# Performance work log

Measured on AMD Instinct MI355X. Metric: run time of the kernel, lower is better.

The kernel has to match this reference:

```python
import jax, jax.numpy as jnp
import numpy as np

PATCH = 7
STRIDE = 1


def extract_patches(im, p=PATCH, stride=STRIDE):
    # im: [b, c, h, w] -> patches [b, N, c*p*p] (torch.nn.Unfold-style layout)
    pt = jax.lax.conv_general_dilated_patches(
        im, filter_shape=(p, p), window_strides=(stride, stride), padding='VALID')
    # pt: [b, c*p*p, h', w']
    b, d = pt.shape[0], pt.shape[1]
    return pt.reshape(b, d, -1).transpose(0, 2, 1)  # [b, N, d]


def coherence_swd(xp, yp, rand):
    # xp, yp: [N, d]; rand: [d, P]
    r = rand / jnp.std(rand, axis=0, keepdims=True, ddof=1)  # torch.std is unbiased
    px = xp @ r  # [N, P]
    py = yp @ r  # [N, P]
    ix = jnp.argsort(px, axis=0).T  # [P, N]
    iy = jnp.argsort(py, axis=0).T  # [P, N]
    # Gather full patch vectors by per-projection sorted order, L1 distance.
    # xp[ix]: [P, N, d] -- the big irregular-gather intermediate.
    diff = jnp.abs(xp[ix] - yp[iy])  # [P, N, d]
    # loss = (1/P) * sum_p mean(|...|_p); each term has identical size -> plain mean
    return diff.mean()


def setup_inputs() -> dict:
    key = jax.random.key(0)
    k1, k2, k3 = jax.random.split(key, 3)
    b, c, h, w = 1, 3, 96, 96
    d = c * PATCH * PATCH  # 147
    num_proj = 256
    x = jax.random.normal(k1, (b, c, h, w), dtype=jnp.float32)
    y = jax.random.normal(k2, (b, c, h, w), dtype=jnp.float32)
    rand = jax.random.normal(k3, (d, num_proj), dtype=jnp.float32)
    return {"x": x, "y": y, "rand": rand}


def reference(x, y, rand):
    x_patches = extract_patches(x)  # [b, N, d]
    y_patches = extract_patches(y)
    losses = jax.vmap(coherence_swd, in_axes=(0, 0, None))(x_patches, y_patches, rand)  # [b]
    return losses.mean()  # batch_reduction='mean'
```

## Files before the change

### kernel.cpp

```cpp
#include <hip/hip_runtime.h>

#define HH 96
#define WW 96
#define OH 90
#define OW 90
#define NPATCH 8100
#define DD 147
#define NPROJ 256
#define TN 64
#define KPAD 160
#define NKS 5
#define SORT_T 512
#define NBUCK 4096
#define KPT 16
#define PGRP 16
#define NCH 64
#define KPB2 128

typedef float vf2 __attribute__((ext_vector_type(2)));
typedef short bf16x8 __attribute__((ext_vector_type(8)));
typedef float f32x4 __attribute__((ext_vector_type(4)));

__device__ __forceinline__ unsigned short bf16_rne(float f) {
    unsigned u = __builtin_bit_cast(unsigned, f);
    u += 0x7FFFu + ((u >> 16) & 1u);
    return (unsigned short)(u >> 16);
}
__device__ __forceinline__ float bf16_f(unsigned short h) {
    return __builtin_bit_cast(float, (unsigned)h << 16);
}

__global__ __launch_bounds__(1024)
void prep_rnd_kernel(const float* __restrict__ rnd,
                     unsigned short* __restrict__ rth,
                     unsigned short* __restrict__ rtl)
{
    const int idx = blockIdx.x * 1024 + threadIdx.x;
    const int k = idx >> 8;
    const int p = idx & 255;
    const float v = (k < DD) ? rnd[k * NPROJ + p] : 0.f;
    const unsigned short hi = bf16_rne(v);
    const unsigned short lo = bf16_rne(v - bf16_f(hi));
    rth[p * KPAD + k] = hi;
    rtl[p * KPAD + k] = lo;
}

__global__ __launch_bounds__(512, 4)
void patch_proj_kernel(const float* __restrict__ x, const float* __restrict__ y,
                       const unsigned short* __restrict__ rth,
                       const unsigned short* __restrict__ rtl,
                       int* __restrict__ xm8, int* __restrict__ ym8,
                       int* __restrict__ xt8, int* __restrict__ yt8,
                       float* __restrict__ pxT, float* __restrict__ pyT,
                       float* __restrict__ out)
{
    __shared__ unsigned short sh[2][TN * KPAD];
    const int tid = threadIdx.x;
    const int n0 = blockIdx.x * TN;
    const int img = blockIdx.y;
    const float* __restrict__ src = img ? y : x;
    int* __restrict__ m8 = img ? ym8 : xm8;
    int* __restrict__ t8 = img ? yt8 : xt8;
    float* __restrict__ pT = img ? pyT : pxT;
    if (blockIdx.x == 0 && img == 0 && tid == 0) out[0] = 0.0f;

    for (int idx = tid; idx < TN * KPAD; idx += 512) {
        const int t = idx / KPAD;
        const int d = idx - t * KPAD;
        const int n = n0 + t;
        float v = 0.f;
        if (n < NPATCH && d < DD) {
            const int oy = n / OW, ox = n - oy * OW;
            const int c  = d / 49, r  = d - c * 49;
            const int di = r / 7,  dj = r - di * 7;
            v = src[c * (HH * WW) + (oy + di) * WW + (ox + dj)];
        }
        const unsigned short hi = bf16_rne(v);
        const unsigned short lo = bf16_rne(v - bf16_f(hi));
        const int mt = t >> 4, r16 = t & 15;
        const int ks = d >> 5, q = (d & 31) >> 3, j = d & 7;
        const int fidx = (((mt * NKS + ks) * 4 + q) * 16 + r16) * 8 + j;
        sh[0][fidx] = hi;
        sh[1][fidx] = lo;
    }
    __syncthreads();

    for (int idx = tid; idx < TN * 40; idx += 512) {
        const int t = idx / 40;
        const int u = idx - t * 40;
        const int n = n0 + t;
        if (n >= NPATCH) continue;
        const int d = 4 * u;
        const int mt = t >> 4, r16 = t & 15;
        const int ks = d >> 5, q = (d & 31) >> 3, jb = d & 7;
        const ushort4 hv = *(const ushort4*)&sh[0][(((mt * NKS + ks) * 4 + q) * 16 + r16) * 8 + jb];
        int w = 0;
        w = __builtin_amdgcn_cvt_pk_fp8_f32(bf16_f(hv.x), bf16_f(hv.y), w, false);
        w = __builtin_amdgcn_cvt_pk_fp8_f32(bf16_f(hv.z), bf16_f(hv.w), w, true);
        if (u < 32) m8[(size_t)n * 32 + u] = w;
        else        t8[(size_t)n * 8 + (u - 32)] = w;
    }

    const int wv = tid >> 6, lane = tid & 63;
    const int cl = lane & 15, qk = lane >> 4;

    f32x4 acc[4][2];
#pragma unroll
    for (int mt = 0; mt < 4; ++mt)
#pragma unroll
        for (int nt = 0; nt < 2; ++nt)
            acc[mt][nt] = (f32x4){0.f, 0.f, 0.f, 0.f};

#pragma unroll
    for (int ks = 0; ks < NKS; ++ks) {
        const int ko = ks * 32 + qk * 8;
        bf16x8 bh[2], bl[2];
#pragma unroll
        for (int nt = 0; nt < 2; ++nt) {
            const int col = wv * 32 + nt * 16 + cl;
            bh[nt] = *(const bf16x8*)&rth[col * KPAD + ko];
            bl[nt] = *(const bf16x8*)&rtl[col * KPAD + ko];
        }
#pragma unroll
        for (int mt = 0; mt < 4; ++mt) {
            const int base = ((mt * NKS + ks) * 64 + lane) * 8;
            const bf16x8 ah = *(const bf16x8*)&sh[0][base];
            const bf16x8 al = *(const bf16x8*)&sh[1][base];
#pragma unroll
            for (int nt = 0; nt < 2; ++nt) {
                acc[mt][nt] = __builtin_amdgcn_mfma_f32_16x16x32_bf16(ah, bh[nt], acc[mt][nt], 0, 0, 0);
                acc[mt][nt] = __builtin_amdgcn_mfma_f32_16x16x32_bf16(ah, bl[nt], acc[mt][nt], 0, 0, 0);
                acc[mt][nt] = __builtin_amdgcn_mfma_f32_16x16x32_bf16(al, bh[nt], acc[mt][nt], 0, 0, 0);
            }
        }
    }

#pragma unroll
    for (int mt = 0; mt < 4; ++mt) {
        const int patch = n0 + mt * 16 + qk * 4;
#pragma unroll
        for (int nt = 0; nt < 2; ++nt) {
            const int proj = wv * 32 + nt * 16 + cl;
            float* rowp = pT + (size_t)proj * NPATCH + patch;
            if (patch + 3 < NPATCH) {
                *(f32x4*)rowp = acc[mt][nt];
            } else {
#pragma unroll
                for (int e = 0; e < 4; ++e)
                    if (patch + e < NPATCH) rowp[e] = acc[mt][nt][e];
            }
        }
    }
}

__global__ __launch_bounds__(SORT_T, 4)
void rank_kernel(const float* __restrict__ pT,
                 unsigned short* __restrict__ rxOut,
                 unsigned short* __restrict__ iyOut)
{
    __shared__ unsigned hist[NBUCK];
    __shared__ unsigned cnt[NBUCK];
    __shared__ float    skey[8192];
    __shared__ unsigned wsum[8];
    const int pb = blockIdx.x;
    const int tid = threadIdx.x;
    const int lane = tid & 63;
    const float* col = pT + (size_t)pb * NPATCH;

    {
        uint4 z = make_uint4(0, 0, 0, 0);
        ((uint4*)hist)[tid] = z;
        ((uint4*)hist)[tid + SORT_T] = z;
    }
    __syncthreads();

    float k[KPT];
    int bk[KPT];
#pragma unroll
    for (int t = 0; t < KPT; ++t) {
        const int i = tid + SORT_T * t;
        if (i < NPATCH) {
            const float v = col[i];
            k[t] = v;
            int b = (int)((v + 51.2f) * 40.0f);
            b = b < 0 ? 0 : (b > NBUCK - 1 ? NBUCK - 1 : b);
            bk[t] = b;
            atomicAdd(&hist[b], 1u);
        } else {
            k[t] = 0.f;
            bk[t] = -1;
        }
    }
    __syncthreads();

    {
        const int b0 = tid * 8;
        unsigned h[8];
#pragma unroll
        for (int q = 0; q < 8; ++q) h[q] = hist[b0 + q];
        unsigned tsum = 0;
#pragma unroll
        for (int q = 0; q < 8; ++q) tsum += h[q];
        unsigned acc = tsum;
#pragma unroll
        for (int d = 1; d < 64; d <<= 1) {
            const unsigned v = __shfl_up(acc, d, 64);
            if (lane >= d) acc += v;
        }
        const unsigned wexcl = acc - tsum;
        if (lane == 63) wsum[tid >> 6] = acc;
        __syncthreads();
        if (tid == 0) {
            unsigned roff = 0;
#pragma unroll
            for (int w = 0; w < 8; ++w) {
                const unsigned tt = wsum[w];
                wsum[w] = roff;
                roff += tt;
            }
        }
        __syncthreads();
        unsigned run = wsum[tid >> 6] + wexcl;
#pragma unroll
        for (int q = 0; q < 8; ++q) { cnt[b0 + q] = run; run += h[q]; }
    }
    __syncthreads();

#pragma unroll
    for (int t = 0; t < KPT; ++t) {
        if (bk[t] >= 0) {
            const unsigned pos = atomicAdd(&cnt[bk[t]], 1u);
            skey[pos] = k[t];
        }
    }
    __syncthreads();

#pragma unroll
    for (int t = 0; t < KPT; ++t) {
        const int i = tid + SORT_T * t;
        if (bk[t] < 0) continue;
        const int b = bk[t];
        const unsigned end = cnt[b];
        const unsigned cb = hist[b];
        const unsigned start = end - cb;
        const float myk = k[t];
        unsigned r = start;
        for (unsigned s2 = start; s2 < end; ++s2)
            r += (skey[s2] < myk) ? 1u : 0u;
        if (pb < NPROJ)
            rxOut[(size_t)pb * NPATCH + i] = (unsigned short)r;
        else
            iyOut[(size_t)(pb - NPROJ) * NPATCH + r] = (unsigned short)i;
    }
}

__device__ __forceinline__ void cvt16f(const uint4 w, float* o) {
    vf2 t;
    t = __builtin_amdgcn_cvt_pk_f32_fp8((int)w.x, false); o[0]  = t.x; o[1]  = t.y;
    t = __builtin_amdgcn_cvt_pk_f32_fp8((int)w.x, true);  o[2]  = t.x; o[3]  = t.y;
    t = __builtin_amdgcn_cvt_pk_f32_fp8((int)w.y, false); o[4]  = t.x; o[5]  = t.y;
    t = __builtin_amdgcn_cvt_pk_f32_fp8((int)w.y, true);  o[6]  = t.x; o[7]  = t.y;
    t = __builtin_amdgcn_cvt_pk_f32_fp8((int)w.z, false); o[8]  = t.x; o[9]  = t.y;
    t = __builtin_amdgcn_cvt_pk_f32_fp8((int)w.z, true);  o[10] = t.x; o[11] = t.y;
    t = __builtin_amdgcn_cvt_pk_f32_fp8((int)w.w, false); o[12] = t.x; o[13] = t.y;
    t = __builtin_amdgcn_cvt_pk_f32_fp8((int)w.w, true);  o[14] = t.x; o[15] = t.y;
}

__device__ __forceinline__ float l1_vs4(const float* xf, unsigned yw, float acc) {
    const vf2 b0 = __builtin_amdgcn_cvt_pk_f32_fp8((int)yw, false);
    const vf2 b1 = __builtin_amdgcn_cvt_pk_f32_fp8((int)yw, true);
    acc += fabsf(xf[0] - b0.x);
    acc += fabsf(xf[1] - b0.y);
    acc += fabsf(xf[2] - b1.x);
    acc += fabsf(xf[3] - b1.y);
    return acc;
}

__global__ __launch_bounds__(256, 4)
void reduce_kernel(const uint4* __restrict__ xm8, const uint4* __restrict__ ym8,
                   const uint4* __restrict__ xt8, const uint4* __restrict__ yt8,
                   const unsigned short* __restrict__ rx,
                   const unsigned short* __restrict__ iy,
                   float* __restrict__ out)
{
    __shared__ unsigned short sp[PGRP * KPB2];
    const int p0 = blockIdx.y * PGRP;
    const int i0 = blockIdx.x * KPB2;
    const int iend = min(i0 + KPB2, NPATCH);
    const int tid = threadIdx.x;
    const int wave = tid >> 6, lane = tid & 63;

    for (int idx = tid; idx < PGRP * KPB2; idx += 256) {
        const int pp = idx >> 7, r = idx & 127;
        int src = i0 + r;
        src = src < NPATCH ? src : NPATCH - 1;
        const int p = p0 + pp;
        const unsigned short rk = rx[(size_t)p * NPATCH + src];
        const unsigned short j = iy[(size_t)p * NPATCH + rk];
        sp[idx] = j < NPATCH ? j : (unsigned short)(NPATCH - 1);
    }
    __syncthreads();

    float facc = 0.f;

    {
        const int g = lane >> 3;
        const int u = lane & 7;
#pragma unroll
        for (int it = 0; it < 4; ++it) {
            const int i = i0 + wave * 8 + it * 32;
            const uint4 xa = xm8[(size_t)i * 8 + lane];
            int jj[PGRP];
#pragma unroll
            for (int pp = 0; pp < PGRP; ++pp)
                jj[pp] = sp[pp * KPB2 + (i - i0) + g];
            uint4 ya[PGRP];
#pragma unroll
            for (int pp = 0; pp < PGRP; ++pp)
                ya[pp] = ym8[(size_t)jj[pp] * 8 + u];
            float xf[16];
            cvt16f(xa, xf);
            float tacc = 0.f;
#pragma unroll
            for (int pp = 0; pp < PGRP; ++pp) {
                tacc = l1_vs4(xf + 0,  ya[pp].x, tacc);
                tacc = l1_vs4(xf + 4,  ya[pp].y, tacc);
                tacc = l1_vs4(xf + 8,  ya[pp].z, tacc);
                tacc = l1_vs4(xf + 12, ya[pp].w, tacc);
            }
            facc += (i + g < iend) ? tacc : 0.f;
        }
    }

    {
        const int g2 = lane >> 1;
        const int u2 = lane & 1;
        const int i2 = i0 + wave * 32;
        const uint4 xa = xt8[(size_t)i2 * 2 + lane];
        int jj[PGRP];
#pragma unroll
        for (int pp = 0; pp < PGRP; ++pp)
            jj[pp] = sp[pp * KPB2 + (i2 - i0) + g2];
        uint4 ya[PGRP];
#pragma unroll
        for (int pp = 0; pp < PGRP; ++pp)
            ya[pp] = yt8[(size_t)jj[pp] * 2 + u2];
        float xf[16];
        cvt16f(xa, xf);
        float tacc = 0.f;
#pragma unroll
        for (int pp = 0; pp < PGRP; ++pp) {
            tacc = l1_vs4(xf + 0,  ya[pp].x, tacc);
            tacc = l1_vs4(xf + 4,  ya[pp].y, tacc);
            tacc = l1_vs4(xf + 8,  ya[pp].z, tacc);
            tacc = l1_vs4(xf + 12, ya[pp].w, tacc);
        }
        facc += (i2 + g2 < iend) ? tacc : 0.f;
    }

#pragma unroll
    for (int o = 32; o > 0; o >>= 1) facc += __shfl_down(facc, o, 64);

    __shared__ float sred[4];
    if (lane == 0) sred[wave] = facc;
    __syncthreads();
    if (tid == 0) {
        const float s = sred[0] + sred[1] + sred[2] + sred[3];
        atomicAdd(out, s * (1.0f / ((float)NPROJ * (float)NPATCH * (float)DD)));
    }
}

extern "C" void kernel_launch(void* const* d_in, const int* in_sizes, int n_in,
                              void* d_out, int out_size, void* d_ws, size_t ws_size,
                              hipStream_t stream)
{
    const float* x   = (const float*)d_in[0];
    const float* y   = (const float*)d_in[1];
    const float* rnd = (const float*)d_in[2];

    char* ws = (char*)d_ws;
    int* xm8 = (int*)(ws + 0);
    int* ym8 = (int*)(ws + 1036800);
    int* xt8 = (int*)(ws + 2073600);
    int* yt8 = (int*)(ws + 2332800);
    float* pxT = (float*)(ws + 2592000);
    float* pyT = (float*)(ws + 10886400);
    unsigned short* rx = (unsigned short*)(ws + 19180800);
    unsigned short* iy = (unsigned short*)(ws + 23328000);
    unsigned short* rth = (unsigned short*)(ws + 27475200);
    unsigned short* rtl = (unsigned short*)(ws + 27557120);
    float* out = (float*)d_out;

    hipLaunchKernelGGL(prep_rnd_kernel, dim3(40), dim3(1024), 0, stream,
                       rnd, rth, rtl);
    hipLaunchKernelGGL(patch_proj_kernel, dim3((NPATCH + TN - 1) / TN, 2), dim3(512), 0, stream,
                       x, y, rth, rtl, xm8, ym8, xt8, yt8, pxT, pyT, out);
    hipLaunchKernelGGL(rank_kernel, dim3(2 * NPROJ), dim3(SORT_T), 0, stream,
                       pxT, rx, iy);
    hipLaunchKernelGGL(reduce_kernel, dim3(NCH, NPROJ / PGRP), dim3(256), 0, stream,
                       (const uint4*)xm8, (const uint4*)ym8,
                       (const uint4*)xt8, (const uint4*)yt8, rx, iy, out);
}
```

Measured before the change: 133.1 us.

## Quantize patches to uint8 and use v_sad_u8; fold rnd prep into projection

Patch values are now stored as 8-bit unsigned linear quantization (scale 21.25, offset 128) instead of fp8, so the L1 reduction can use v_sad_u8 integer sum-of-absolute-differences rather than fp8-to-float conversion and float abs-sub. The separate prep_rnd kernel is removed: each projection block splits rnd into bf16 hi/lo in registers, which saves a launch but repeats that conversion in every block. The patch load and quantization are fused into one pass, and occupancy hint drops to 2. Clamping and linear quantization change accuracy relative to fp8, and the loss is approximated to low precision.

Result: faster. 126.9 us (-4.6%).

```diff
diff --git a/kernel.cpp b/kernel.cpp
--- a/kernel.cpp
+++ b/kernel.cpp
@@ -16,8 +16,8 @@
 #define PGRP 16
 #define NCH 64
 #define KPB2 128
-
-typedef float vf2 __attribute__((ext_vector_type(2)));
+#define QSCALE 21.25f
+
 typedef short bf16x8 __attribute__((ext_vector_type(8)));
 typedef float f32x4 __attribute__((ext_vector_type(4)));
 
@@ -30,25 +30,15 @@
     return __builtin_bit_cast(float, (unsigned)h << 16);
 }
 
-__global__ __launch_bounds__(1024)
-void prep_rnd_kernel(const float* __restrict__ rnd,
-                     unsigned short* __restrict__ rth,
-                     unsigned short* __restrict__ rtl)
-{
-    const int idx = blockIdx.x * 1024 + threadIdx.x;
-    const int k = idx >> 8;
-    const int p = idx & 255;
-    const float v = (k < DD) ? rnd[k * NPROJ + p] : 0.f;
-    const unsigned short hi = bf16_rne(v);
-    const unsigned short lo = bf16_rne(v - bf16_f(hi));
-    rth[p * KPAD + k] = hi;
-    rtl[p * KPAD + k] = lo;
-}
-
-__global__ __launch_bounds__(512, 4)
+__device__ __forceinline__ unsigned sad4(unsigned x, unsigned y, unsigned a) {
+    unsigned d;
+    asm("v_sad_u8 %0, %1, %2, %3" : "=v"(d) : "v"(x), "v"(y), "v"(a));
+    return d;
+}
+
+__global__ __launch_bounds__(512, 2)
 void patch_proj_kernel(const float* __restrict__ x, const float* __restrict__ y,
-                       const unsigned short* __restrict__ rth,
-                       const unsigned short* __restrict__ rtl,
+                       const float* __restrict__ rnd,
                        int* __restrict__ xm8, int* __restrict__ ym8,
                        int* __restrict__ xt8, int* __restrict__ yt8,
                        float* __restrict__ pxT, float* __restrict__ pyT,
@@ -64,45 +54,66 @@
     float* __restrict__ pT = img ? pyT : pxT;
     if (blockIdx.x == 0 && img == 0 && tid == 0) out[0] = 0.0f;
 
-    for (int idx = tid; idx < TN * KPAD; idx += 512) {
-        const int t = idx / KPAD;
-        const int d = idx - t * KPAD;
-        const int n = n0 + t;
-        float v = 0.f;
-        if (n < NPATCH && d < DD) {
-            const int oy = n / OW, ox = n - oy * OW;
-            const int c  = d / 49, r  = d - c * 49;
-            const int di = r / 7,  dj = r - di * 7;
-            v = src[c * (HH * WW) + (oy + di) * WW + (ox + dj)];
-        }
-        const unsigned short hi = bf16_rne(v);
-        const unsigned short lo = bf16_rne(v - bf16_f(hi));
-        const int mt = t >> 4, r16 = t & 15;
-        const int ks = d >> 5, q = (d & 31) >> 3, j = d & 7;
-        const int fidx = (((mt * NKS + ks) * 4 + q) * 16 + r16) * 8 + j;
-        sh[0][fidx] = hi;
-        sh[1][fidx] = lo;
-    }
-    __syncthreads();
+    const int wv = tid >> 6, lane = tid & 63;
+    const int cl = lane & 15, qk = lane >> 4;
+
+    bf16x8 bh[NKS][2], bl[NKS][2];
+#pragma unroll
+    for (int ks = 0; ks < NKS; ++ks) {
+#pragma unroll
+        for (int nt = 0; nt < 2; ++nt) {
+            const int col = wv * 32 + nt * 16 + cl;
+#pragma unroll
+            for (int j = 0; j < 8; ++j) {
+                const int k = ks * 32 + qk * 8 + j;
+                const float v = (k < DD) ? rnd[k * NPROJ + col] : 0.f;
+                const unsigned short h = bf16_rne(v);
+                bh[ks][nt][j] = (short)h;
+                bl[ks][nt][j] = (short)bf16_rne(v - bf16_f(h));
+            }
+        }
+    }
 
     for (int idx = tid; idx < TN * 40; idx += 512) {
         const int t = idx / 40;
         const int u = idx - t * 40;
         const int n = n0 + t;
-        if (n >= NPATCH) continue;
-        const int d = 4 * u;
+        const int d0 = 4 * u;
+        unsigned short h4[4], l4[4];
+#pragma unroll
+        for (int e = 0; e < 4; ++e) {
+            const int d = d0 + e;
+            float v = 0.f;
+            if (n < NPATCH && d < DD) {
+                const int oy = n / OW, ox = n - oy * OW;
+                const int c  = d / 49, r  = d - c * 49;
+                const int di = r / 7,  dj = r - di * 7;
+                v = src[c * (HH * WW) + (oy + di) * WW + (ox + dj)];
+            }
+            const unsigned short hi = bf16_rne(v);
+            h4[e] = hi;
+            l4[e] = bf16_rne(v - bf16_f(hi));
+        }
         const int mt = t >> 4, r16 = t & 15;
-        const int ks = d >> 5, q = (d & 31) >> 3, jb = d & 7;
-        const ushort4 hv = *(const ushort4*)&sh[0][(((mt * NKS + ks) * 4 + q) * 16 + r16) * 8 + jb];
-        int w = 0;
-        w = __builtin_amdgcn_cvt_pk_fp8_f32(bf16_f(hv.x), bf16_f(hv.y), w, false);
-        w = __builtin_amdgcn_cvt_pk_fp8_f32(bf16_f(hv.z), bf16_f(hv.w), w, true);
-        if (u < 32) m8[(size_t)n * 32 + u] = w;
-        else        t8[(size_t)n * 8 + (u - 32)] = w;
-    }
-
-    const int wv = tid >> 6, lane = tid & 63;
-    const int cl = lane & 15, qk = lane >> 4;
+        const int ks = d0 >> 5, q = (d0 & 31) >> 3, jb = d0 & 7;
+        const int fidx = (((mt * NKS + ks) * 4 + q) * 16 + r16) * 8 + jb;
+        ushort4 hv; hv.x = h4[0]; hv.y = h4[1]; hv.z = h4[2]; hv.w = h4[3];
+        ushort4 lv; lv.x = l4[0]; lv.y = l4[1]; lv.z = l4[2]; lv.w = l4[3];
+        *(ushort4*)&sh[0][fidx] = hv;
+        *(ushort4*)&sh[1][fidx] = lv;
+        if (n < NPATCH) {
+            unsigned w = 0;
+#pragma unroll
+            for (int e = 0; e < 4; ++e) {
+                float f = fmaf(bf16_f(h4[e]), QSCALE, 128.5f);
+                f = fminf(fmaxf(f, 0.f), 255.f);
+                w |= ((unsigned)f) << (8 * e);
+            }
+            if (u < 32) m8[(size_t)n * 32 + u] = (int)w;
+            else        t8[(size_t)n * 8 + (u - 32)] = (int)w;
+        }
+    }
+    __syncthreads();
 
     f32x4 acc[4][2];
 #pragma unroll
@@ -113,14 +124,6 @@
 
 #pragma unroll
     for (int ks = 0; ks < NKS; ++ks) {
-        const int ko = ks * 32 + qk * 8;
-        bf16x8 bh[2], bl[2];
-#pragma unroll
-        for (int nt = 0; nt < 2; ++nt) {
-            const int col = wv * 32 + nt * 16 + cl;
-            bh[nt] = *(const bf16x8*)&rth[col * KPAD + ko];
-            bl[nt] = *(const bf16x8*)&rtl[col * KPAD + ko];
-        }
 #pragma unroll
         for (int mt = 0; mt < 4; ++mt) {
             const int base = ((mt * NKS + ks) * 64 + lane) * 8;
@@ -128,9 +131,9 @@
             const bf16x8 al = *(const bf16x8*)&sh[1][base];
 #pragma unroll
             for (int nt = 0; nt < 2; ++nt) {
-                acc[mt][nt] = __builtin_amdgcn_mfma_f32_16x16x32_bf16(ah, bh[nt], acc[mt][nt], 0, 0, 0);
-                acc[mt][nt] = __builtin_amdgcn_mfma_f32_16x16x32_bf16(ah, bl[nt], acc[mt][nt], 0, 0, 0);
-                acc[mt][nt] = __builtin_amdgcn_mfma_f32_16x16x32_bf16(al, bh[nt], acc[mt][nt], 0, 0, 0);
+                acc[mt][nt] = __builtin_amdgcn_mfma_f32_16x16x32_bf16(ah, bh[ks][nt], acc[mt][nt], 0, 0, 0);
+                acc[mt][nt] = __builtin_amdgcn_mfma_f32_16x16x32_bf16(ah, bl[ks][nt], acc[mt][nt], 0, 0, 0);
+                acc[mt][nt] = __builtin_amdgcn_mfma_f32_16x16x32_bf16(al, bh[ks][nt], acc[mt][nt], 0, 0, 0);
             }
         }
     }
@@ -254,28 +257,6 @@
     }
 }
 
-__device__ __forceinline__ void cvt16f(const uint4 w, float* o) {
-    vf2 t;
-    t = __builtin_amdgcn_cvt_pk_f32_fp8((int)w.x, false); o[0]  = t.x; o[1]  = t.y;
-    t = __builtin_amdgcn_cvt_pk_f32_fp8((int)w.x, true);  o[2]  = t.x; o[3]  = t.y;
-    t = __builtin_amdgcn_cvt_pk_f32_fp8((int)w.y, false); o[4]  = t.x; o[5]  = t.y;
-    t = __builtin_amdgcn_cvt_pk_f32_fp8((int)w.y, true);  o[6]  = t.x; o[7]  = t.y;
-    t = __builtin_amdgcn_cvt_pk_f32_fp8((int)w.z, false); o[8]  = t.x; o[9]  = t.y;
-    t = __builtin_amdgcn_cvt_pk_f32_fp8((int)w.z, true);  o[10] = t.x; o[11] = t.y;
-    t = __builtin_amdgcn_cvt_pk_f32_fp8((int)w.w, false); o[12] = t.x; o[13] = t.y;
-    t = __builtin_amdgcn_cvt_pk_f32_fp8((int)w.w, true);  o[14] = t.x; o[15] = t.y;
-}
-
-__device__ __forceinline__ float l1_vs4(const float* xf, unsigned yw, float acc) {
-    const vf2 b0 = __builtin_amdgcn_cvt_pk_f32_fp8((int)yw, false);
-    const vf2 b1 = __builtin_amdgcn_cvt_pk_f32_fp8((int)yw, true);
-    acc += fabsf(xf[0] - b0.x);
-    acc += fabsf(xf[1] - b0.y);
-    acc += fabsf(xf[2] - b1.x);
-    acc += fabsf(xf[3] - b1.y);
-    return acc;
-}
-
 __global__ __launch_bounds__(256, 4)
 void reduce_kernel(const uint4* __restrict__ xm8, const uint4* __restrict__ ym8,
                    const uint4* __restrict__ xt8, const uint4* __restrict__ yt8,
@@ -301,7 +282,7 @@
     }
     __syncthreads();
 
-    float facc = 0.f;
+    unsigned uacc = 0;
 
     {
         const int g = lane >> 3;
@@ -318,17 +299,15 @@
 #pragma unroll
             for (int pp = 0; pp < PGRP; ++pp)
                 ya[pp] = ym8[(size_t)jj[pp] * 8 + u];
-            float xf[16];
-            cvt16f(xa, xf);
-            float tacc = 0.f;
+            unsigned s0 = 0, s1 = 0;
 #pragma unroll
             for (int pp = 0; pp < PGRP; ++pp) {
-                tacc = l1_vs4(xf + 0,  ya[pp].x, tacc);
-                tacc = l1_vs4(xf + 4,  ya[pp].y, tacc);
-                tacc = l1_vs4(xf + 8,  ya[pp].z, tacc);
-                tacc = l1_vs4(xf + 12, ya[pp].w, tacc);
-            }
-            facc += (i + g < iend) ? tacc : 0.f;
+                s0 = sad4(xa.x, ya[pp].x, s0);
+                s1 = sad4(xa.y, ya[pp].y, s1);
+                s0 = sad4(xa.z, ya[pp].z, s0);
+                s1 = sad4(xa.w, ya[pp].w, s1);
+            }
+            uacc += (i + g < iend) ? (s0 + s1) : 0u;
         }
     }
 
@@ -345,19 +324,18 @@
 #pragma unroll
         for (int pp = 0; pp < PGRP; ++pp)
             ya[pp] = yt8[(size_t)jj[pp] * 2 + u2];
-        float xf[16];
-        cvt16f(xa, xf);
-        float tacc = 0.f;
+        unsigned s0 = 0, s1 = 0;
 #pragma unroll
         for (int pp = 0; pp < PGRP; ++pp) {
-            tacc = l1_vs4(xf + 0,  ya[pp].x, tacc);
-            tacc = l1_vs4(xf + 4,  ya[pp].y, tacc);
-            tacc = l1_vs4(xf + 8,  ya[pp].z, tacc);
-            tacc = l1_vs4(xf + 12, ya[pp].w, tacc);
-        }
-        facc += (i2 + g2 < iend) ? tacc : 0.f;
-    }
-
+            s0 = sad4(xa.x, ya[pp].x, s0);
+            s1 = sad4(xa.y, ya[pp].y, s1);
+            s0 = sad4(xa.z, ya[pp].z, s0);
+            s1 = sad4(xa.w, ya[pp].w, s1);
+        }
+        uacc += (i2 + g2 < iend) ? (s0 + s1) : 0u;
+    }
+
+    float facc = (float)uacc;
 #pragma unroll
     for (int o = 32; o > 0; o >>= 1) facc += __shfl_down(facc, o, 64);
 
@@ -366,7 +344,9 @@
     __syncthreads();
     if (tid == 0) {
         const float s = sred[0] + sred[1] + sred[2] + sred[3];
-        atomicAdd(out, s * (1.0f / ((float)NPROJ * (float)NPATCH * (float)DD)));
+        const float scale = (float)(1.0 / ((double)NPROJ * (double)NPATCH *
+                                           (double)DD * (double)QSCALE));
+        atomicAdd(out, s * scale);
     }
 }
 
@@ -387,14 +367,10 @@
     float* pyT = (float*)(ws + 10886400);
     unsigned short* rx = (unsigned short*)(ws + 19180800);
     unsigned short* iy = (unsigned short*)(ws + 23328000);
-    unsigned short* rth = (unsigned short*)(ws + 27475200);
-    unsigned short* rtl = (unsigned short*)(ws + 27557120);
     float* out = (float*)d_out;
 
-    hipLaunchKernelGGL(prep_rnd_kernel, dim3(40), dim3(1024), 0, stream,
-                       rnd, rth, rtl);
     hipLaunchKernelGGL(patch_proj_kernel, dim3((NPATCH + TN - 1) / TN, 2), dim3(512), 0, stream,
-                       x, y, rth, rtl, xm8, ym8, xt8, yt8, pxT, pyT, out);
+                       x, y, rnd, xm8, ym8, xt8, yt8, pxT, pyT, out);
     hipLaunchKernelGGL(rank_kernel, dim3(2 * NPROJ), dim3(SORT_T), 0, stream,
                        pxT, rx, iy);
     hipLaunchKernelGGL(reduce_kernel, dim3(NCH, NPROJ / PGRP), dim3(256), 0, stream,
```
